# Kernel optimization log

Measured on AMD Instinct MI355X. Metric: run time of the kernel, lower is better.

Reference implementation:

```python
import jax, jax.numpy as jnp
import numpy as np


def setup_inputs() -> dict:
    key = jax.random.key(0)
    ks = jax.random.split(key, 8)
    C = 128
    Cq = C // 8  # 16
    x = jax.random.normal(ks[0], (4, C, 64, 64), dtype=jnp.float32)
    s = 1.0 / np.sqrt(C)
    wq = jax.random.normal(ks[1], (Cq, C), dtype=jnp.float32) * s
    bq = jnp.zeros((Cq,), dtype=jnp.float32)
    wk = jax.random.normal(ks[2], (Cq, C), dtype=jnp.float32) * s
    bk = jnp.zeros((Cq,), dtype=jnp.float32)
    wv = jax.random.normal(ks[3], (C, C), dtype=jnp.float32) * s
    bv = jnp.zeros((C,), dtype=jnp.float32)
    gamma = jnp.array([0.5], dtype=jnp.float32)
    return {"x": x, "wq": wq, "bq": bq, "wk": wk, "bk": bk,
            "wv": wv, "bv": bv, "gamma": gamma}


def reference(x, wq, bq, wk, bk, wv, bv, gamma):
    B, C, W, H = x.shape
    N = W * H
    xf = x.reshape(B, C, N)  # flatten spatial; 1x1 conv == channel matmul
    q = jnp.einsum('qc,bcn->bnq', wq, xf) + bq[None, None, :]  # B,N,Cq
    k = jnp.einsum('qc,bcn->bqn', wk, xf) + bk[None, :, None]  # B,Cq,N
    v = jnp.einsum('vc,bcn->bvn', wv, xf) + bv[None, :, None]  # B,C,N
    energy = jnp.einsum('bnq,bqm->bnm', q, k)                  # B,N,N (no scaling)
    attention = jax.nn.softmax(energy, axis=-1)
    out = jnp.einsum('bvm,bnm->bvn', v, attention)             # V @ A^T
    out = out.reshape(B, C, W, H)
    return gamma[0] * out + x
```

## Files before the change

kernel.cpp:

```cpp
#include <hip/hip_runtime.h>

#define B_    4
#define C_    128
#define CQ_   16
#define N_    4096
#define SPLIT 4
#define MPER  (N_ / SPLIT)
#define KVBLK 64

typedef short          s16x8 __attribute__((ext_vector_type(8)));
typedef unsigned short u16x4 __attribute__((ext_vector_type(4)));
typedef unsigned int   u32x4 __attribute__((ext_vector_type(4)));
typedef float          f32x4 __attribute__((ext_vector_type(4)));
typedef unsigned short u16;
typedef unsigned int   u32;

__device__ __forceinline__ u16 f2bf(float f) {
    unsigned int u = __builtin_bit_cast(unsigned int, f);
    u += 0x7fffu + ((u >> 16) & 1u);
    return (u16)(u >> 16);
}
__device__ __forceinline__ float bf2f(u16 h) {
    unsigned int u = ((unsigned int)h) << 16;
    return __builtin_bit_cast(float, u);
}
__device__ __forceinline__ s16x8 ld8bf(const u16* p) {
    return *reinterpret_cast<const s16x8*>(p);
}
__device__ __forceinline__ u32 cvtpk_bf16(float lo, float hi) {
    u32 r;
    asm("v_cvt_pk_bf16_f32 %0, %1, %2" : "=v"(r) : "v"(lo), "v"(hi));
    return r;
}
__device__ __forceinline__ void gld_lds16(const u16* src, u16* lds) {
    __builtin_amdgcn_global_load_lds(
        (const __attribute__((address_space(1))) void*)src,
        (__attribute__((address_space(3))) void*)lds, 16, 0, 0);
}

__global__ __launch_bounds__(256) void proj_all_kernel(
    const float* __restrict__ x,
    const float* __restrict__ wq, const float* __restrict__ bq,
    const float* __restrict__ wk, const float* __restrict__ bk,
    const float* __restrict__ wv, const float* __restrict__ bv,
    u16* __restrict__ Qb, u16* __restrict__ Kb, u16* __restrict__ Vb)
{
    __shared__ float smem[12800];
    const int tid = threadIdx.x;
    const int b   = blockIdx.y;
    const int nl  = tid & 63;
    const int n   = blockIdx.x * 64 + nl;
    const int ch  = tid >> 6;
    const float* xp = x + ((size_t)b * C_) * N_ + n;

    if (blockIdx.z == 0) {
        float* wqs = smem;
        float* wks = smem + 2048;
        float (*part)[4][64][17] = (float (*)[4][64][17])(smem + 4096);
        for (int i = tid; i < CQ_ * C_; i += 256) { wqs[i] = wq[i]; wks[i] = wk[i]; }
        __syncthreads();

        float qa[CQ_], ka[CQ_];
#pragma unroll
        for (int j = 0; j < CQ_; ++j) { qa[j] = 0.f; ka[j] = 0.f; }
        const int c0 = ch * 32;
        for (int c = c0; c < c0 + 32; ++c) {
            const float xv = xp[(size_t)c * N_];
#pragma unroll
            for (int j = 0; j < CQ_; ++j) {
                qa[j] = fmaf(wqs[j * C_ + c], xv, qa[j]);
                ka[j] = fmaf(wks[j * C_ + c], xv, ka[j]);
            }
        }
#pragma unroll
        for (int j = 0; j < CQ_; ++j) { part[0][ch][nl][j] = qa[j]; part[1][ch][nl][j] = ka[j]; }
        __syncthreads();

        if (tid < 128) {
            const int which = tid >> 6;
            const int n2 = tid & 63;
            const float* bias = which ? bk : bq;
            alignas(16) u16 row[32];
#pragma unroll
            for (int j = 0; j < CQ_; ++j) {
                float v = part[which][0][n2][j] + part[which][1][n2][j]
                        + part[which][2][n2][j] + part[which][3][n2][j] + bias[j];
                u16 h = f2bf(v);
                row[j]       = h;
                row[CQ_ + j] = f2bf(v - bf2f(h));
            }
            u16* dst = (which ? Kb : Qb) + ((size_t)(b * N_ + blockIdx.x * 64 + n2)) * 32;
#pragma unroll
            for (int i = 0; i < 4; ++i)
                reinterpret_cast<uint4*>(dst)[i] = reinterpret_cast<const uint4*>(row)[i];
        }
    } else {
        const int cv0 = (blockIdx.z - 1) * 32;
        float* wvs = smem;
        float (*part)[64][33] = (float (*)[64][33])(smem + 4096);
        for (int i = tid; i < 32 * C_; i += 256) wvs[i] = wv[cv0 * C_ + i];
        __syncthreads();

        float acc[32];
#pragma unroll
        for (int j = 0; j < 32; ++j) acc[j] = 0.f;
        const int c0 = ch * 32;
        for (int c = c0; c < c0 + 32; ++c) {
            const float xv = xp[(size_t)c * N_];
#pragma unroll
            for (int j = 0; j < 32; ++j) acc[j] = fmaf(wvs[j * C_ + c], xv, acc[j]);
        }
#pragma unroll
        for (int j = 0; j < 32; ++j) part[ch][nl][j] = acc[j];
        __syncthreads();

        const int jq = tid >> 6;
#pragma unroll
        for (int jj = 0; jj < 8; ++jj) {
            const int j = jq * 8 + jj;
            float v = part[0][nl][j] + part[1][nl][j] + part[2][nl][j] + part[3][nl][j]
                    + bv[cv0 + j];
            Vb[((size_t)(b * C_ + cv0 + j)) * N_ + blockIdx.x * 64 + nl] = f2bf(v);
        }
    }
}

__global__ __launch_bounds__(256, 4) void attn_split_kernel(
    const u16* __restrict__ Qb, const u16* __restrict__ Kb, const u16* __restrict__ Vb,
    u16* __restrict__ Opart, float* __restrict__ Lpart)
{
    __shared__ __align__(16) u16 Kt[2][KVBLK * 32];
    __shared__ __align__(16) u16 Vt[2][C_ * KVBLK];

    const int tid  = threadIdx.x;
    const int lane = tid & 63;
    const int l16  = lane & 15;
    const int g    = lane >> 4;
    const int wave = tid >> 6;
    const int b    = blockIdx.y;
    const int n0   = blockIdx.x * 64;
    const int s    = blockIdx.z;
    const int ms   = s * MPER;

    const int qn = n0 + wave * 16 + l16;
    const s16x8 qf = ld8bf(Qb + ((size_t)(b * N_ + qn)) * 32 + 8 * g);

    const int kv_s   = tid >> 2;
    const int kcol_s = ((tid & 3) * 16) ^ ((kv_s & 3) << 4);
    const u16* ksrc0 = Kb + ((size_t)b * N_ + kv_s) * 32 + (kcol_s >> 1);
    const int vc_s   = tid >> 3;
    const u16* vsrc0[4];
#pragma unroll
    for (int i = 0; i < 4; ++i) {
        const int c_i  = i * 32 + vc_s;
        const int vcol = ((tid & 7) * 16) ^ ((c_i & 7) << 4);
        vsrc0[i] = Vb + ((size_t)(b * C_ + c_i)) * N_ + (vcol >> 1);
    }

    const bool hig = (g >= 2);
    const bool mid = (g == 1) || (g == 2);

    f32x4 acc[8];
#pragma unroll
    for (int cg = 0; cg < 8; ++cg) acc[cg] = {};
    float lpart = 0.f;

    gld_lds16(ksrc0 + (size_t)ms * 32, &Kt[0][wave * 512]);
#pragma unroll
    for (int i = 0; i < 4; ++i)
        gld_lds16(vsrc0[i] + ms, &Vt[0][i * 2048 + wave * 512]);
    asm volatile("s_waitcnt vmcnt(0)" ::: "memory");
    __syncthreads();

    int cur = 0;
    for (int t = 0; t < MPER / KVBLK; ++t) {
        if (t + 1 < MPER / KVBLK) {
            const int mn = ms + (t + 1) * KVBLK;
            gld_lds16(ksrc0 + (size_t)mn * 32, &Kt[cur ^ 1][wave * 512]);
#pragma unroll
            for (int i = 0; i < 4; ++i)
                gld_lds16(vsrc0[i] + mn, &Vt[cur ^ 1][i * 2048 + wave * 512]);
        }

        const u16* ktb = &Kt[cur][0];
        f32x4 sacc[4];
#pragma unroll
        for (int mg = 0; mg < 4; ++mg) {
            const int kv  = 16 * mg + l16;
            const int swz = (kv & 3) << 4;
            const s16x8 kf1 = ld8bf(ktb + kv * 32 + (((16 * (g & 1)) ^ swz) >> 1));
            s16x8 kf2 = {};
            if (g < 2) kf2 = ld8bf(ktb + kv * 32 + (((32 + 16 * g) ^ swz) >> 1));
            f32x4 z = {};
            z = __builtin_amdgcn_mfma_f32_16x16x32_bf16(kf1, qf, z, 0, 0, 0);
            z = __builtin_amdgcn_mfma_f32_16x16x32_bf16(kf2, qf, z, 0, 0, 0);
            sacc[mg] = z;
        }

        float p[4][4];
#pragma unroll
        for (int mg = 0; mg < 4; ++mg) {
#pragma unroll
            for (int i = 0; i < 4; ++i) {
                p[mg][i] = __expf(sacc[mg][i]);
                lpart += p[mg][i];
            }
        }

        const u16* vtb = &Vt[cur][0];
        const int vswz = (l16 & 7) << 4;
#pragma unroll
        for (int ss = 0; ss < 2; ++ss) {
            const u32 a0 = cvtpk_bf16(p[2 * ss][0],     p[2 * ss][1]);
            const u32 b0 = cvtpk_bf16(p[2 * ss][2],     p[2 * ss][3]);
            const u32 a1 = cvtpk_bf16(p[2 * ss + 1][0], p[2 * ss + 1][1]);
            const u32 b1 = cvtpk_bf16(p[2 * ss + 1][2], p[2 * ss + 1][3]);

            const u32 mA = (u32)__shfl_xor((int)(hig ? a0 : a1), 32);
            const u32 mB = (u32)__shfl_xor((int)(hig ? b0 : b1), 32);
            const u32 oA = hig ? a1 : a0;
            const u32 oB = hig ? b1 : b0;
            const u32 eA = mid ? mA : oA;
            const u32 eB = mid ? mB : oB;
            const u32 vA = mid ? oA : mA;
            const u32 vB = mid ? oB : mB;
            const u32 xA = (u32)__shfl_xor((int)vA, 16);
            const u32 xB = (u32)__shfl_xor((int)vB, 16);
            u32x4 w;
            w[0] = (g & 1) ? xA : eA;
            w[1] = (g & 1) ? xB : eB;
            w[2] = (g & 1) ? eA : xA;
            w[3] = (g & 1) ? eB : xB;
            const s16x8 pf = __builtin_bit_cast(s16x8, w);
            const int vcol = (64 * ss + 16 * g) ^ vswz;
#pragma unroll
            for (int cg = 0; cg < 8; ++cg) {
                const int c = 16 * cg + l16;
                const s16x8 vf = ld8bf(vtb + c * 64 + (vcol >> 1));
                acc[cg] = __builtin_amdgcn_mfma_f32_16x16x32_bf16(vf, pf, acc[cg], 0, 0, 0);
            }
        }

        asm volatile("s_waitcnt vmcnt(0)" ::: "memory");
        __syncthreads();
        cur ^= 1;
    }

    lpart += __shfl_xor(lpart, 16);
    lpart += __shfl_xor(lpart, 32);
    const size_t sb = (size_t)(s * B_ + b);
    if (lane < 16) Lpart[sb * N_ + n0 + wave * 16 + l16] = lpart;

    const int n = n0 + wave * 16 + l16;
#pragma unroll
    for (int cg = 0; cg < 8; ++cg) {
#pragma unroll
        for (int i = 0; i < 4; ++i) {
            const int c = 16 * cg + 4 * g + i;
            Opart[(sb * C_ + c) * N_ + n] = f2bf(acc[cg][i]);
        }
    }
}

__global__ __launch_bounds__(256) void reduce_kernel(
    const u16* __restrict__ Opart, const float* __restrict__ Lpart,
    const float* __restrict__ x, const float* __restrict__ gamma,
    float* __restrict__ out)
{
    const int t  = blockIdx.x * 256 + threadIdx.x;
    const size_t e0 = (size_t)t * 4;
    const int n = (int)(e0 & (N_ - 1));
    const int c = (int)((e0 >> 12) & (C_ - 1));
    const int b = (int)(e0 >> 19);

    float o0 = 0.f, o1 = 0.f, o2 = 0.f, o3 = 0.f;
    f32x4 l = {};
#pragma unroll
    for (int s = 0; s < SPLIT; ++s) {
        const size_t sb = (size_t)(s * B_ + b);
        const u16x4 ov = *reinterpret_cast<const u16x4*>(Opart + (sb * C_ + c) * N_ + n);
        const f32x4 lv = *reinterpret_cast<const f32x4*>(Lpart + sb * N_ + n);
        o0 += bf2f(ov[0]); o1 += bf2f(ov[1]); o2 += bf2f(ov[2]); o3 += bf2f(ov[3]);
        l += lv;
    }
    const float gm = gamma[0];
    const f32x4 xv = *reinterpret_cast<const f32x4*>(x + e0);
    f32x4 r;
    r[0] = gm * o0 / l[0] + xv[0];
    r[1] = gm * o1 / l[1] + xv[1];
    r[2] = gm * o2 / l[2] + xv[2];
    r[3] = gm * o3 / l[3] + xv[3];
    *reinterpret_cast<f32x4*>(out + e0) = r;
}

extern "C" void kernel_launch(void* const* d_in, const int* in_sizes, int n_in,
                              void* d_out, int out_size, void* d_ws, size_t ws_size,
                              hipStream_t stream)
{
    const float* x     = (const float*)d_in[0];
    const float* wq    = (const float*)d_in[1];
    const float* bq    = (const float*)d_in[2];
    const float* wk    = (const float*)d_in[3];
    const float* bk    = (const float*)d_in[4];
    const float* wv    = (const float*)d_in[5];
    const float* bv    = (const float*)d_in[6];
    const float* gamma = (const float*)d_in[7];
    float* out = (float*)d_out;

    u16* Qb = (u16*)d_ws;
    u16* Kb = Qb + (size_t)B_ * N_ * 32;
    u16* Vb = Kb + (size_t)B_ * N_ * 32;
    u16* Opart = Vb + (size_t)B_ * C_ * N_;
    float* Lpart = (float*)(Opart + (size_t)SPLIT * B_ * C_ * N_);

    proj_all_kernel<<<dim3(N_ / 64, B_, 5), 256, 0, stream>>>(
        x, wq, bq, wk, bk, wv, bv, Qb, Kb, Vb);
    attn_split_kernel<<<dim3(N_ / 64, B_, SPLIT), 256, 0, stream>>>(
        Qb, Kb, Vb, Opart, Lpart);
    reduce_kernel<<<(B_ * C_ * N_ / 4) / 256, 256, 0, stream>>>(
        Opart, Lpart, x, gamma, out);
}
```

Measured before the change: 78.73 us.

## Process two query tiles per wave to reuse K/V LDS fragments

Each block now handles 128 queries instead of 64, with each wave computing two 16-row query tiles. Every K and V fragment read from LDS feeds two MFMAs, which halves LDS traffic and global K/V loads per query. It also adds s_setprio around the MFMA sections, precomputed swizzle offsets, and a manually unrolled double-buffer loop. In exchange it doubles accumulator registers (launch bounds lowered to 2 blocks per SM) and halves the grid size, which risks lower occupancy and poorer load balance.

```diff
diff --git a/kernel.cpp b/kernel.cpp
--- a/kernel.cpp
+++ b/kernel.cpp
@@ -7,6 +7,7 @@
 #define SPLIT 4
 #define MPER  (N_ / SPLIT)
 #define KVBLK 64
+#define NT    (MPER / KVBLK)
 
 typedef short          s16x8 __attribute__((ext_vector_type(8)));
 typedef unsigned short u16x4 __attribute__((ext_vector_type(4)));
@@ -125,7 +126,7 @@
     }
 }
 
-__global__ __launch_bounds__(256, 4) void attn_split_kernel(
+__global__ __launch_bounds__(256, 2) void attn_split_kernel(
     const u16* __restrict__ Qb, const u16* __restrict__ Kb, const u16* __restrict__ Vb,
     u16* __restrict__ Opart, float* __restrict__ Lpart)
 {
@@ -138,12 +139,13 @@
     const int g    = lane >> 4;
     const int wave = tid >> 6;
     const int b    = blockIdx.y;
-    const int n0   = blockIdx.x * 64;
+    const int n0   = blockIdx.x * 128;
     const int s    = blockIdx.z;
     const int ms   = s * MPER;
 
-    const int qn = n0 + wave * 16 + l16;
-    const s16x8 qf = ld8bf(Qb + ((size_t)(b * N_ + qn)) * 32 + 8 * g);
+    const int qn = n0 + wave * 32 + l16;
+    const s16x8 qf0 = ld8bf(Qb + ((size_t)(b * N_ + qn)) * 32 + 8 * g);
+    const s16x8 qf1 = ld8bf(Qb + ((size_t)(b * N_ + qn + 16)) * 32 + 8 * g);
 
     const int kv_s   = tid >> 2;
     const int kcol_s = ((tid & 3) * 16) ^ ((kv_s & 3) << 4);
@@ -157,13 +159,104 @@
         vsrc0[i] = Vb + ((size_t)(b * C_ + c_i)) * N_ + (vcol >> 1);
     }
 
+    const int kswz  = (l16 & 3) << 4;
+    const int vswz  = (l16 & 7) << 4;
+    const int koff1 = l16 * 32 + (((16 * (g & 1)) ^ kswz) >> 1);
+    const int koff2 = l16 * 32 + (((32 + 16 * g) ^ kswz) >> 1);
+    const int voffA = l16 * 64 + (((16 * g) ^ vswz) >> 1);
+    const int voffB = l16 * 64 + (((64 + 16 * g) ^ vswz) >> 1);
+
     const bool hig = (g >= 2);
     const bool mid = (g == 1) || (g == 2);
 
-    f32x4 acc[8];
-#pragma unroll
-    for (int cg = 0; cg < 8; ++cg) acc[cg] = {};
-    float lpart = 0.f;
+    f32x4 acc0[8], acc1[8];
+#pragma unroll
+    for (int cg = 0; cg < 8; ++cg) { acc0[cg] = {}; acc1[cg] = {}; }
+    float lp0 = 0.f, lp1 = 0.f;
+
+    auto relayout = [&](const float (&p)[4][4], int ss) -> s16x8 {
+        const u32 a0 = cvtpk_bf16(p[2 * ss][0],     p[2 * ss][1]);
+        const u32 b0 = cvtpk_bf16(p[2 * ss][2],     p[2 * ss][3]);
+        const u32 a1 = cvtpk_bf16(p[2 * ss + 1][0], p[2 * ss + 1][1]);
+        const u32 b1 = cvtpk_bf16(p[2 * ss + 1][2], p[2 * ss + 1][3]);
+        const u32 mA = (u32)__shfl_xor((int)(hig ? a0 : a1), 32);
+        const u32 mB = (u32)__shfl_xor((int)(hig ? b0 : b1), 32);
+        const u32 oA = hig ? a1 : a0;
+        const u32 oB = hig ? b1 : b0;
+        const u32 eA = mid ? mA : oA;
+        const u32 eB = mid ? mB : oB;
+        const u32 vA = mid ? oA : mA;
+        const u32 vB = mid ? oB : mB;
+        const u32 xA = (u32)__shfl_xor((int)vA, 16);
+        const u32 xB = (u32)__shfl_xor((int)vB, 16);
+        u32x4 w;
+        w[0] = (g & 1) ? xA : eA;
+        w[1] = (g & 1) ? xB : eB;
+        w[2] = (g & 1) ? eA : xA;
+        w[3] = (g & 1) ? eB : xB;
+        return __builtin_bit_cast(s16x8, w);
+    };
+
+    auto body = [&](int t, int buf) {
+        if (t + 1 < NT) {
+            const int mn = ms + (t + 1) * KVBLK;
+            gld_lds16(ksrc0 + (size_t)mn * 32, &Kt[buf ^ 1][wave * 512]);
+#pragma unroll
+            for (int i = 0; i < 4; ++i)
+                gld_lds16(vsrc0[i] + mn, &Vt[buf ^ 1][i * 2048 + wave * 512]);
+        }
+        const u16* ktb = &Kt[buf][0];
+        const u16* vtb = &Vt[buf][0];
+
+        f32x4 s0[4], s1[4];
+        __builtin_amdgcn_s_setprio(1);
+#pragma unroll
+        for (int mg = 0; mg < 4; ++mg) {
+            const s16x8 kf1 = ld8bf(ktb + koff1 + mg * 512);
+            s16x8 kf2 = {};
+            if (g < 2) kf2 = ld8bf(ktb + koff2 + mg * 512);
+            f32x4 z0 = {}, z1 = {};
+            z0 = __builtin_amdgcn_mfma_f32_16x16x32_bf16(kf1, qf0, z0, 0, 0, 0);
+            z0 = __builtin_amdgcn_mfma_f32_16x16x32_bf16(kf2, qf0, z0, 0, 0, 0);
+            z1 = __builtin_amdgcn_mfma_f32_16x16x32_bf16(kf1, qf1, z1, 0, 0, 0);
+            z1 = __builtin_amdgcn_mfma_f32_16x16x32_bf16(kf2, qf1, z1, 0, 0, 0);
+            s0[mg] = z0; s1[mg] = z1;
+        }
+        __builtin_amdgcn_s_setprio(0);
+
+        s16x8 pf00, pf01, pf10, pf11;
+        {
+            float p[4][4];
+#pragma unroll
+            for (int mg = 0; mg < 4; ++mg)
+#pragma unroll
+                for (int i = 0; i < 4; ++i) { p[mg][i] = __expf(s0[mg][i]); lp0 += p[mg][i]; }
+            pf00 = relayout(p, 0); pf01 = relayout(p, 1);
+        }
+        {
+            float p[4][4];
+#pragma unroll
+            for (int mg = 0; mg < 4; ++mg)
+#pragma unroll
+                for (int i = 0; i < 4; ++i) { p[mg][i] = __expf(s1[mg][i]); lp1 += p[mg][i]; }
+            pf10 = relayout(p, 0); pf11 = relayout(p, 1);
+        }
+
+        __builtin_amdgcn_s_setprio(1);
+#pragma unroll
+        for (int cg = 0; cg < 8; ++cg) {
+            const s16x8 vfa = ld8bf(vtb + voffA + cg * 1024);
+            acc0[cg] = __builtin_amdgcn_mfma_f32_16x16x32_bf16(vfa, pf00, acc0[cg], 0, 0, 0);
+            acc1[cg] = __builtin_amdgcn_mfma_f32_16x16x32_bf16(vfa, pf10, acc1[cg], 0, 0, 0);
+            const s16x8 vfb = ld8bf(vtb + voffB + cg * 1024);
+            acc0[cg] = __builtin_amdgcn_mfma_f32_16x16x32_bf16(vfb, pf01, acc0[cg], 0, 0, 0);
+            acc1[cg] = __builtin_amdgcn_mfma_f32_16x16x32_bf16(vfb, pf11, acc1[cg], 0, 0, 0);
+        }
+        __builtin_amdgcn_s_setprio(0);
+
+        asm volatile("s_waitcnt vmcnt(0)" ::: "memory");
+        __syncthreads();
+    };
 
     gld_lds16(ksrc0 + (size_t)ms * 32, &Kt[0][wave * 512]);
 #pragma unroll
@@ -172,92 +265,27 @@
     asm volatile("s_waitcnt vmcnt(0)" ::: "memory");
     __syncthreads();
 
-    int cur = 0;
-    for (int t = 0; t < MPER / KVBLK; ++t) {
-        if (t + 1 < MPER / KVBLK) {
-            const int mn = ms + (t + 1) * KVBLK;
-            gld_lds16(ksrc0 + (size_t)mn * 32, &Kt[cur ^ 1][wave * 512]);
-#pragma unroll
-            for (int i = 0; i < 4; ++i)
-                gld_lds16(vsrc0[i] + mn, &Vt[cur ^ 1][i * 2048 + wave * 512]);
-        }
-
-        const u16* ktb = &Kt[cur][0];
-        f32x4 sacc[4];
-#pragma unroll
-        for (int mg = 0; mg < 4; ++mg) {
-            const int kv  = 16 * mg + l16;
-            const int swz = (kv & 3) << 4;
-            const s16x8 kf1 = ld8bf(ktb + kv * 32 + (((16 * (g & 1)) ^ swz) >> 1));
-            s16x8 kf2 = {};
-            if (g < 2) kf2 = ld8bf(ktb + kv * 32 + (((32 + 16 * g) ^ swz) >> 1));
-            f32x4 z = {};
-            z = __builtin_amdgcn_mfma_f32_16x16x32_bf16(kf1, qf, z, 0, 0, 0);
-            z = __builtin_amdgcn_mfma_f32_16x16x32_bf16(kf2, qf, z, 0, 0, 0);
-            sacc[mg] = z;
-        }
-
-        float p[4][4];
-#pragma unroll
-        for (int mg = 0; mg < 4; ++mg) {
-#pragma unroll
-            for (int i = 0; i < 4; ++i) {
-                p[mg][i] = __expf(sacc[mg][i]);
-                lpart += p[mg][i];
-            }
-        }
-
-        const u16* vtb = &Vt[cur][0];
-        const int vswz = (l16 & 7) << 4;
-#pragma unroll
-        for (int ss = 0; ss < 2; ++ss) {
-            const u32 a0 = cvtpk_bf16(p[2 * ss][0],     p[2 * ss][1]);
-            const u32 b0 = cvtpk_bf16(p[2 * ss][2],     p[2 * ss][3]);
-            const u32 a1 = cvtpk_bf16(p[2 * ss + 1][0], p[2 * ss + 1][1]);
-            const u32 b1 = cvtpk_bf16(p[2 * ss + 1][2], p[2 * ss + 1][3]);
-
-            const u32 mA = (u32)__shfl_xor((int)(hig ? a0 : a1), 32);
-            const u32 mB = (u32)__shfl_xor((int)(hig ? b0 : b1), 32);
-            const u32 oA = hig ? a1 : a0;
-            const u32 oB = hig ? b1 : b0;
-            const u32 eA = mid ? mA : oA;
-            const u32 eB = mid ? mB : oB;
-            const u32 vA = mid ? oA : mA;
-            const u32 vB = mid ? oB : mB;
-            const u32 xA = (u32)__shfl_xor((int)vA, 16);
-            const u32 xB = (u32)__shfl_xor((int)vB, 16);
-            u32x4 w;
-            w[0] = (g & 1) ? xA : eA;
-            w[1] = (g & 1) ? xB : eB;
-            w[2] = (g & 1) ? eA : xA;
-            w[3] = (g & 1) ? eB : xB;
-            const s16x8 pf = __builtin_bit_cast(s16x8, w);
-            const int vcol = (64 * ss + 16 * g) ^ vswz;
-#pragma unroll
-            for (int cg = 0; cg < 8; ++cg) {
-                const int c = 16 * cg + l16;
-                const s16x8 vf = ld8bf(vtb + c * 64 + (vcol >> 1));
-                acc[cg] = __builtin_amdgcn_mfma_f32_16x16x32_bf16(vf, pf, acc[cg], 0, 0, 0);
-            }
-        }
-
-        asm volatile("s_waitcnt vmcnt(0)" ::: "memory");
-        __syncthreads();
-        cur ^= 1;
-    }
-
-    lpart += __shfl_xor(lpart, 16);
-    lpart += __shfl_xor(lpart, 32);
+    for (int tt = 0; tt < NT / 2; ++tt) {
+        body(2 * tt, 0);
+        body(2 * tt + 1, 1);
+    }
+
+    lp0 += __shfl_xor(lp0, 16);  lp0 += __shfl_xor(lp0, 32);
+    lp1 += __shfl_xor(lp1, 16);  lp1 += __shfl_xor(lp1, 32);
     const size_t sb = (size_t)(s * B_ + b);
-    if (lane < 16) Lpart[sb * N_ + n0 + wave * 16 + l16] = lpart;
-
-    const int n = n0 + wave * 16 + l16;
+    if (lane < 16) {
+        Lpart[sb * N_ + n0 + wave * 32 + l16]      = lp0;
+        Lpart[sb * N_ + n0 + wave * 32 + 16 + l16] = lp1;
+    }
+
+    const int na = n0 + wave * 32 + l16;
 #pragma unroll
     for (int cg = 0; cg < 8; ++cg) {
 #pragma unroll
         for (int i = 0; i < 4; ++i) {
             const int c = 16 * cg + 4 * g + i;
-            Opart[(sb * C_ + c) * N_ + n] = f2bf(acc[cg][i]);
+            Opart[(sb * C_ + c) * N_ + na]      = f2bf(acc0[cg][i]);
+            Opart[(sb * C_ + c) * N_ + na + 16] = f2bf(acc1[cg][i]);
         }
     }
 }
@@ -315,7 +343,7 @@
 
     proj_all_kernel<<<dim3(N_ / 64, B_, 5), 256, 0, stream>>>(
         x, wq, bq, wk, bk, wv, bv, Qb, Kb, Vb);
-    attn_split_kernel<<<dim3(N_ / 64, B_, SPLIT), 256, 0, stream>>>(
+    attn_split_kernel<<<dim3(N_ / 128, B_, SPLIT), 256, 0, stream>>>(
         Qb, Kb, Vb, Opart, Lpart);
     reduce_kernel<<<(B_ * C_ * N_ / 4) / 256, 256, 0, stream>>>(
         Opart, Lpart, x, gamma, out);
```

New measurement: 74.65 us. -5.2%, faster.
